# Kernel optimization log

Hardware: AMD Instinct MI355X
Metric: run time of the kernel (lower is better)

## Reference

```python
import jax, jax.numpy as jnp
import numpy as np


def median_pool8(x):
    # x: (N, 1, H0, W0); 8x8 non-overlapping blocks, lower median (torch.median semantics)
    N, C, H0, W0 = x.shape
    H, W = H0 // 8, W0 // 8
    blocks = x.reshape(N, C, H, 8, W, 8).transpose(0, 1, 2, 4, 3, 5).reshape(N, C, H, W, 64)
    return jnp.sort(blocks, axis=-1)[..., (64 - 1) // 2]


def prelu(x, a):
    return jnp.where(x >= 0, x, a * x)


def setup_inputs() -> dict:
    key = jax.random.key(0)
    ks = jax.random.split(key, 12)
    N, C, H, W = 8, 128, 45, 60
    s = 0.05
    return {
        "cnn_encoder_output": jax.random.normal(ks[0], (N, C, H, W), jnp.float32),
        "original_input": jax.random.uniform(ks[1], (N, 4, H * 8, W * 8), jnp.float32),
        "xy": jax.random.normal(ks[2], (N, 2, H * 8, W * 8), jnp.float32),
        # g MLP: two Linear(128,128) + PReLU (single alpha each)
        "g_w0": jax.random.normal(ks[3], (C, C), jnp.float32) * s,
        "g_b0": jnp.zeros((C,), jnp.float32),
        "g_a0": jnp.full((1,), 0.25, jnp.float32),
        "g_w1": jax.random.normal(ks[4], (C, C), jnp.float32) * s,
        "g_b1": jnp.zeros((C,), jnp.float32),
        "g_a1": jnp.full((1,), 0.25, jnp.float32),
        # q update: Linear(256,128) + PReLU
        "q_w": jax.random.normal(ks[5], (C, 2 * C), jnp.float32) * s,
        "q_b": jnp.zeros((C,), jnp.float32),
        "q_a": jnp.full((1,), 0.25, jnp.float32),
        # output conv: Conv2d(256, 128, 3, padding=1)
        "conv_w": jax.random.normal(ks[6], (C, 2 * C, 3, 3), jnp.float32) * s,
        "conv_b": jnp.zeros((C,), jnp.float32),
        "gnn_iterations": 2,
        "k": 16,
        "use_half_precision": 0,
    }


def reference(cnn_encoder_output, original_input, xy,
              g_w0, g_b0, g_a0, g_w1, g_b1, g_a1,
              q_w, q_b, q_a, conv_w, conv_b,
              gnn_iterations, k, use_half_precision):
    N, C, H, W = cnn_encoder_output.shape
    HW = H * W

    # 3D projection: median-pooled x, y, depth -> (N, HW, 3)
    depth = median_pool8(original_input[:, 3:4])
    xc = median_pool8(xy[:, 0:1])
    yc = median_pool8(xy[:, 1:2])
    proj = jnp.concatenate([xc, yc, depth], axis=1).reshape(N, 3, HW).transpose(0, 2, 1)

    # batched KNN: D_ij = sqrt(|pi|^2 + |pj|^2 - 2 pi.pj), k smallest per row
    sq = jnp.sum(proj * proj, axis=-1)                        # (N, HW)
    r = jnp.einsum('nic,njc->nij', proj, proj)                # (N, HW, HW)
    D = jnp.sqrt(jnp.maximum(sq[:, :, None] + sq[:, None, :] - 2.0 * r, 0.0))
    _, knn = jax.lax.top_k(-D, k)                             # (N, HW, K) indices

    h = cnn_encoder_output.transpose(0, 2, 3, 1).reshape(N, HW, C)
    g_params = [(g_w0, g_b0, g_a0), (g_w1, g_b1, g_a1)]

    for _ in range(gnn_iterations):
        # gather neighbor features: (N, HW, K, C)
        nf = jax.vmap(lambda hn, kn: hn[kn])(h, knn)
        for w, b, a in g_params:
            nf = prelu(nf @ w.T + b, a)
        m = jnp.mean(nf, axis=2)                              # (N, HW, C)
        h = prelu(jnp.concatenate([h, m], axis=-1) @ q_w.T + q_b, q_a)

    h_img = h.reshape(N, H, W, C).transpose(0, 3, 1, 2)
    inp = jnp.concatenate([cnn_encoder_output, h_img], axis=1)  # (N, 2C, H, W)
    out = jax.lax.conv_general_dilated(
        inp, conv_w, window_strides=(1, 1), padding=((1, 1), (1, 1)),
        dimension_numbers=('NCHW', 'OIHW', 'NCHW')) + conv_b[None, :, None, None]
    return out
```

## Files before the change

kernel.cpp:

```cpp
#include <hip/hip_runtime.h>
#include <cfloat>
#include <cmath>

#define NB 8
#define CC 128
#define HH 45
#define WW 60
#define HWP 2700
#define KNN 16
#define H0 360
#define W0 480
#define NT 43
#define MROWS 21600

typedef __bf16 bf16_8 __attribute__((ext_vector_type(8)));
typedef __bf16 bf16_4 __attribute__((ext_vector_type(4)));
typedef float  f32x4  __attribute__((ext_vector_type(4)));

__global__ void transpose_cl(const float* __restrict__ in, float* __restrict__ out) {
    __shared__ float tile[32][33];
    int n = blockIdx.z;
    int c0 = blockIdx.y * 32;
    int p0 = blockIdx.x * 32;
    int tx = threadIdx.x & 31, ty = threadIdx.x >> 5;
    #pragma unroll
    for (int r = 0; r < 32; r += 8) {
        int c = c0 + ty + r, p = p0 + tx;
        tile[ty + r][tx] = (p < HWP) ? in[((size_t)n * CC + c) * HWP + p] : 0.f;
    }
    __syncthreads();
    #pragma unroll
    for (int r = 0; r < 32; r += 8) {
        int p = p0 + ty + r, c = c0 + tx;
        if (p < HWP) out[((size_t)n * HWP + p) * CC + c] = tile[tx][ty + r];
    }
}

__global__ void median_pool(const float* __restrict__ xy, const float* __restrict__ orig,
                            float* __restrict__ proj) {
    int w = blockIdx.x * 4 + (threadIdx.x >> 6);
    int lane = threadIdx.x & 63;
    int n = w / (3 * HWP);
    int rem = w % (3 * HWP);
    int c = rem / HWP;
    int b = rem % HWP;
    const float* src = (c < 2) ? (xy + ((size_t)n * 2 + c) * H0 * W0)
                               : (orig + ((size_t)n * 4 + 3) * H0 * W0);
    int by = b / WW, bx = b % WW;
    int r = lane >> 3, col = lane & 7;
    float v = src[(by * 8 + r) * W0 + bx * 8 + col];
    #pragma unroll
    for (int k = 2; k <= 64; k <<= 1) {
        #pragma unroll
        for (int j2 = k >> 1; j2 >= 1; j2 >>= 1) {
            float p = __shfl_xor(v, j2, 64);
            bool dir = (lane & k) == 0;
            bool low = (lane & j2) == 0;
            v = (dir == low) ? fminf(v, p) : fmaxf(v, p);
        }
    }
    if (lane == 31) proj[(size_t)c * (NB * HWP) + (size_t)n * HWP + b] = v;
}

__global__ void __launch_bounds__(512, 6) knn_kernel(const float* __restrict__ proj,
                                                     int* __restrict__ knn) {
#pragma clang fp contract(off)
    __shared__ float4 pts[HWP];
    __shared__ int sbufj[8][64];
    int n = blockIdx.y;
    const float* px = proj + (size_t)n * HWP;
    const float* py = proj + (size_t)NB * HWP + (size_t)n * HWP;
    const float* pz = proj + (size_t)2 * NB * HWP + (size_t)n * HWP;
    for (int t = threadIdx.x; t < HWP; t += 512) {
        float x = px[t], y = py[t], z = pz[t];
        float4 p;
        p.x = x; p.y = y; p.z = z;
        p.w = (x * x + y * y) + z * z;
        pts[t] = p;
    }
    __syncthreads();

    int wave = threadIdx.x >> 6;
    int lane = threadIdx.x & 63;
    int i = blockIdx.x * 8 + wave;
    if (i >= HWP) return;
    float4 pi = pts[i];
    float xi = pi.x, yi = pi.y, zi = pi.z, sqi = pi.w;

    unsigned int sdp[22];
    float mn = FLT_MAX;
    #pragma unroll
    for (int t = 0; t < NT; ++t) {
        int j = lane + t * 64;
        unsigned int u = 0xFFFFu;
        if (j < HWP) {
            float4 pj = pts[j];
            float r = fmaf(zi, pj.z, fmaf(yi, pj.y, xi * pj.x));
            float s = (sqi + pj.w) - 2.0f * r;
            mn = fminf(mn, s);
            float sc = fmaxf(s, 0.f);
            u = (__float_as_uint(sc) + 0xFFFFu) >> 16;
        }
        if (t & 1) sdp[t >> 1] |= (u << 16);
        else       sdp[t >> 1] = u;
    }

    float v = mn;
    #pragma unroll
    for (int k = 2; k <= 64; k <<= 1) {
        #pragma unroll
        for (int j2 = k >> 1; j2 >= 1; j2 >>= 1) {
            float p = __shfl_xor(v, j2, 64);
            bool dir = (lane & k) == 0;
            bool low = (lane & j2) == 0;
            v = (dir == low) ? fminf(v, p) : fmaxf(v, p);
        }
    }
    float M_s = __shfl(v, 15, 64);
    float M_test = (M_s > 0.f) ? (M_s * 1.0000005f + 1e-37f) : 0.0f;
    float M_t2 = M_test * 1.009f;
    unsigned int M_bits = __float_as_uint(M_t2);

    int cnt = 0;
    #pragma unroll
    for (int t = 0; t < NT; ++t) {
        unsigned int u = (t & 1) ? (sdp[t >> 1] >> 16) : (sdp[t >> 1] & 0xFFFFu);
        bool pred = (u << 16) <= M_bits;
        unsigned long long b = __ballot(pred);
        if (b) {
            int off = cnt + (int)__popcll(b & ((1ull << lane) - 1ull));
            if (pred && off < 64) sbufj[wave][off] = lane + t * 64;
            cnt += (int)__popcll(b);
        }
    }

    int myj = 0;
    if (cnt >= KNN && cnt <= 64) {
        unsigned long long key = ~0ull;
        if (lane < cnt) {
            int j = sbufj[wave][lane];
            float4 pj = pts[j];
            float r = fmaf(zi, pj.z, fmaf(yi, pj.y, xi * pj.x));
            float s = (sqi + pj.w) - 2.0f * r;
            float d = sqrtf(fmaxf(s, 0.f));
            key = ((unsigned long long)__float_as_uint(d) << 32) | (unsigned int)j;
        }
        #pragma unroll
        for (int k = 2; k <= 64; k <<= 1) {
            #pragma unroll
            for (int j2 = k >> 1; j2 >= 1; j2 >>= 1) {
                unsigned long long p = __shfl_xor(key, j2, 64);
                bool dir = (lane & k) == 0;
                bool low = (lane & j2) == 0;
                bool keepmin = (dir == low);
                bool pless = p < key;
                key = (pless == keepmin) ? p : key;
            }
        }
        myj = (int)(unsigned int)(key & 0xffffffffull);
    } else {
        float lastd = -FLT_MAX; int lastj = -1;
        #pragma unroll 1
        for (int r = 0; r < KNN; ++r) {
            float bd = FLT_MAX; int bj = 0x7fffffff;
            #pragma unroll 1
            for (int t = 0; t < NT; ++t) {
                int j = lane + t * 64;
                if (j < HWP) {
                    float4 pj = pts[j];
                    float rr = fmaf(zi, pj.z, fmaf(yi, pj.y, xi * pj.x));
                    float s = (sqi + pj.w) - 2.0f * rr;
                    float d = sqrtf(fmaxf(s, 0.f));
                    bool gt = (d > lastd) || (d == lastd && j > lastj);
                    bool lt = (d < bd) || (d == bd && j < bj);
                    if (gt && lt) { bd = d; bj = j; }
                }
            }
            float md = bd; int mj = bj;
            #pragma unroll
            for (int off = 32; off >= 1; off >>= 1) {
                float od = __shfl_xor(md, off, 64);
                int oj = __shfl_xor(mj, off, 64);
                if (od < md || (od == md && oj < mj)) { md = od; mj = oj; }
            }
            if (lane == r) myj = mj;
            lastd = md; lastj = mj;
        }
    }
    if (lane < KNN)
        knn[((size_t)n * HWP + i) * KNN + lane] = myj;
}

template <int K>
__device__ __forceinline__ void wsplit_body(const float* __restrict__ Wt,
                                            __bf16* __restrict__ wh,
                                            __bf16* __restrict__ wl,
                                            int bx, int tid) {
    int t = bx * 256 + tid;
    int j = t & 7;
    int lane = (t >> 3) & 63;
    int nt = (t >> 9) & 7;
    int kc = t >> 12;
    int oc = nt * 16 + (lane & 15);
    int k = kc * 32 + (lane >> 4) * 8 + j;
    float v = Wt[(size_t)oc * K + k];
    __bf16 hi = (__bf16)v;
    wh[t] = hi;
    wl[t] = (__bf16)(v - (float)hi);
}

__global__ void prep_all(const float* __restrict__ g_w0, const float* __restrict__ g_w1,
                         const float* __restrict__ q_w, const float* __restrict__ conv_w,
                         __bf16* __restrict__ g0h, __bf16* __restrict__ g0l,
                         __bf16* __restrict__ g1h, __bf16* __restrict__ g1l,
                         __bf16* __restrict__ qh, __bf16* __restrict__ ql,
                         __bf16* __restrict__ w_frag) {
    int bx = blockIdx.x, tid = threadIdx.x;
    if (bx < 64)        wsplit_body<128>(g_w0, g0h, g0l, bx, tid);
    else if (bx < 128)  wsplit_body<128>(g_w1, g1h, g1l, bx - 64, tid);
    else if (bx < 256)  wsplit_body<256>(q_w, qh, ql, bx - 128, tid);
    else {
        int t = (bx - 256) * 256 + tid;
        int j = t & 7;
        int lane = (t >> 3) & 63;
        int ntile = (t >> 9) & 7;
        int icc = (t >> 12) & 7;
        int tap = t >> 15;
        int oc = ntile * 16 + (lane & 15);
        int ic = icc * 32 + (lane >> 4) * 8 + j;
        w_frag[t] = (__bf16)conv_w[((size_t)oc * 256 + ic) * 9 + tap];
    }
}

__device__ __forceinline__ void layer_32x128(
    const float* __restrict__ src,
    const __bf16* __restrict__ wh, const __bf16* __restrict__ wl,
    int wave, int lane, int kc_base, f32x4 acc[2][2]) {
    int quad = lane >> 4, lm = lane & 15;
    const bf16_8* wh8 = (const bf16_8*)wh;
    const bf16_8* wl8 = (const bf16_8*)wl;
    #pragma unroll
    for (int kc = 0; kc < 4; ++kc) {
        bf16_8 bh[2], bl[2];
        #pragma unroll
        for (int nt = 0; nt < 2; ++nt) {
            const float* p = &src[(nt * 16 + lm) * 132 + kc * 32 + quad * 8];
            float4 v0 = *(const float4*)p;
            float4 v1 = *(const float4*)(p + 4);
            float vs[8] = {v0.x, v0.y, v0.z, v0.w, v1.x, v1.y, v1.z, v1.w};
            #pragma unroll
            for (int e = 0; e < 8; ++e) {
                __bf16 hi = (__bf16)vs[e];
                bh[nt][e] = hi;
                bl[nt][e] = (__bf16)(vs[e] - (float)hi);
            }
        }
        bf16_8 ah[2], al[2];
        #pragma unroll
        for (int mt = 0; mt < 2; ++mt) {
            size_t idx = ((size_t)(kc_base + kc) * 8 + (wave * 2 + mt)) * 64 + lane;
            ah[mt] = wh8[idx];
            al[mt] = wl8[idx];
        }
        #pragma unroll
        for (int mt = 0; mt < 2; ++mt)
            #pragma unroll
            for (int nt = 0; nt < 2; ++nt) {
                acc[mt][nt] = __builtin_amdgcn_mfma_f32_16x16x32_bf16(ah[mt], bh[nt], acc[mt][nt], 0, 0, 0);
                acc[mt][nt] = __builtin_amdgcn_mfma_f32_16x16x32_bf16(ah[mt], bl[nt], acc[mt][nt], 0, 0, 0);
                acc[mt][nt] = __builtin_amdgcn_mfma_f32_16x16x32_bf16(al[mt], bh[nt], acc[mt][nt], 0, 0, 0);
            }
    }
}

__global__ void __launch_bounds__(256) fused_g(
    const float* __restrict__ Ain,
    const __bf16* __restrict__ w0h, const __bf16* __restrict__ w0l,
    const float* __restrict__ b0, const float* __restrict__ a0p,
    const __bf16* __restrict__ w1h, const __bf16* __restrict__ w1l,
    const float* __restrict__ b1, const float* __restrict__ a1p,
    __bf16* __restrict__ tgb) {
    __shared__ float albuf[32 * 132];
    __shared__ float inter[32 * 132];
    int r0 = blockIdx.x * 32;
    int tid = threadIdx.x;
    int wave = tid >> 6, lane = tid & 63;
    int quad = lane >> 4, lm = lane & 15;
    for (int t = tid; t < 1024; t += 256) {
        int row = t >> 5, c4 = (t & 31) * 4;
        *(float4*)&albuf[row * 132 + c4] = *(const float4*)&Ain[(size_t)(r0 + row) * 128 + c4];
    }
    __syncthreads();
    {
        f32x4 acc[2][2] = {};
        layer_32x128(albuf, w0h, w0l, wave, lane, 0, acc);
        float alpha = a0p[0];
        #pragma unroll
        for (int mt = 0; mt < 2; ++mt) {
            int oc0 = wave * 32 + mt * 16 + quad * 4;
            float4 bb = *(const float4*)&b0[oc0];
            float bv[4] = {bb.x, bb.y, bb.z, bb.w};
            #pragma unroll
            for (int nt = 0; nt < 2; ++nt) {
                float4 o;
                float* op = (float*)&o;
                #pragma unroll
                for (int reg = 0; reg < 4; ++reg) {
                    float vv = acc[mt][nt][reg] + bv[reg];
                    op[reg] = (vv >= 0.f) ? vv : alpha * vv;
                }
                *(float4*)&inter[(nt * 16 + lm) * 132 + oc0] = o;
            }
        }
    }
    __syncthreads();
    {
        f32x4 acc[2][2] = {};
        layer_32x128(inter, w1h, w1l, wave, lane, 0, acc);
        float alpha = a1p[0];
        #pragma unroll
        for (int mt = 0; mt < 2; ++mt) {
            int oc0 = wave * 32 + mt * 16 + quad * 4;
            float4 bb = *(const float4*)&b1[oc0];
            float bv[4] = {bb.x, bb.y, bb.z, bb.w};
            #pragma unroll
            for (int nt = 0; nt < 2; ++nt) {
                bf16_4 o;
                #pragma unroll
                for (int reg = 0; reg < 4; ++reg) {
                    float vv = acc[mt][nt][reg] + bv[reg];
                    vv = (vv >= 0.f) ? vv : alpha * vv;
                    o[reg] = (__bf16)vv;
                }
                *(bf16_4*)&tgb[(size_t)(r0 + nt * 16 + lm) * 128 + oc0] = o;
            }
        }
    }
}

__global__ void __launch_bounds__(256) fused_q(
    const float* __restrict__ Ain, const __bf16* __restrict__ tgb,
    const int* __restrict__ knn_idx,
    const __bf16* __restrict__ qh, const __bf16* __restrict__ ql,
    const float* __restrict__ qb, const float* __restrict__ qap,
    float* __restrict__ hout) {
    __shared__ float hlds[32 * 132];
    __shared__ float mlds[32 * 132];
    int r0 = blockIdx.x * 32;
    int tid = threadIdx.x;
    int wave = tid >> 6, lane = tid & 63;
    int quad = lane >> 4, lm = lane & 15;
    for (int t = tid; t < 1024; t += 256) {
        int row = t >> 5, c4 = (t & 31) * 4;
        *(float4*)&hlds[row * 132 + c4] = *(const float4*)&Ain[(size_t)(r0 + row) * 128 + c4];
    }
    {
        int pix = tid >> 3;
        int oct0 = (tid & 7) * 2;
        int grow = r0 + pix;
        int nimg = grow / HWP;
        const int* kn = knn_idx + (size_t)grow * KNN;
        const __bf16* tbase = tgb + ((size_t)nimg * HWP) * 128;
        float a0[8] = {}, a1[8] = {};
        #pragma unroll
        for (int k = 0; k < KNN; ++k) {
            int j = kn[k];
            const __bf16* srcp = tbase + (size_t)j * 128 + oct0 * 8;
            bf16_8 v0 = *(const bf16_8*)srcp;
            bf16_8 v1 = *(const bf16_8*)(srcp + 8);
            #pragma unroll
            for (int e = 0; e < 8; ++e) { a0[e] += (float)v0[e]; a1[e] += (float)v1[e]; }
        }
        const float s = 1.f / 16.f;
        float* dst = &mlds[pix * 132 + oct0 * 8];
        float4 o0 = {a0[0] * s, a0[1] * s, a0[2] * s, a0[3] * s};
        float4 o1 = {a0[4] * s, a0[5] * s, a0[6] * s, a0[7] * s};
        float4 o2 = {a1[0] * s, a1[1] * s, a1[2] * s, a1[3] * s};
        float4 o3 = {a1[4] * s, a1[5] * s, a1[6] * s, a1[7] * s};
        *(float4*)(dst) = o0; *(float4*)(dst + 4) = o1;
        *(float4*)(dst + 8) = o2; *(float4*)(dst + 12) = o3;
    }
    __syncthreads();
    f32x4 acc[2][2] = {};
    layer_32x128(hlds, qh, ql, wave, lane, 0, acc);
    layer_32x128(mlds, qh, ql, wave, lane, 4, acc);
    float alpha = qap[0];
    #pragma unroll
    for (int mt = 0; mt < 2; ++mt) {
        int oc0 = wave * 32 + mt * 16 + quad * 4;
        float4 bb = *(const float4*)&qb[oc0];
        float bv[4] = {bb.x, bb.y, bb.z, bb.w};
        #pragma unroll
        for (int nt = 0; nt < 2; ++nt) {
            float4 o;
            float* op = (float*)&o;
            #pragma unroll
            for (int reg = 0; reg < 4; ++reg) {
                float vv = acc[mt][nt][reg] + bv[reg];
                op[reg] = (vv >= 0.f) ? vv : alpha * vv;
            }
            *(float4*)&hout[(size_t)(r0 + nt * 16 + lm) * 128 + oc0] = o;
        }
    }
}

__global__ void pack_input(const float* __restrict__ cnn_cl, const float* __restrict__ h,
                           __bf16* __restrict__ pad_in) {
    int t = blockIdx.x * 256 + threadIdx.x;
    int cg = t & 31;
    int s = t >> 5;
    int q = s % 68; s /= 68;
    int p = s % 47;
    int n = s / 47;
    int y = p - 1, x = q - 1;
    bf16_8 v = {};
    if (y >= 0 && y < HH && x >= 0 && x < WW) {
        int c0 = cg * 8;
        const float* src = (c0 < 128)
            ? (cnn_cl + (((size_t)n * HWP + y * WW + x) * 128 + c0))
            : (h      + (((size_t)n * HWP + y * WW + x) * 128 + (c0 - 128)));
        float4 l0 = *(const float4*)&src[0];
        float4 l1 = *(const float4*)&src[4];
        v[0] = (__bf16)l0.x; v[1] = (__bf16)l0.y; v[2] = (__bf16)l0.z; v[3] = (__bf16)l0.w;
        v[4] = (__bf16)l1.x; v[5] = (__bf16)l1.y; v[6] = (__bf16)l1.z; v[7] = (__bf16)l1.w;
    }
    ((bf16_8*)pad_in)[t] = v;
}

__global__ void __launch_bounds__(256) conv_mfma(
    const __bf16* __restrict__ pad_in,
    const __bf16* __restrict__ w_frag,
    const float* __restrict__ bias,
    float* __restrict__ out) {
    __shared__ __bf16 alds[3 * 66 * 32];
    int y = blockIdx.x;
    int oh = blockIdx.y;
    int n = blockIdx.z;
    int tid = threadIdx.x;
    int wave = tid >> 6, lane = tid & 63;
    int wm = wave & 1, wq = wave >> 1;
    int quad = lane >> 4, lm = lane & 15;

    f32x4 acc[2][2] = {};
    const bf16_8* wf = (const bf16_8*)w_frag;

    for (int icc = 0; icc < 8; ++icc) {
        __syncthreads();
        for (int t = tid; t < 792; t += 256) {
            int cq = t & 3;
            int xp = (t >> 2) % 66;
            int dy = (t >> 2) / 66;
            size_t src = (((size_t)n * 47 + (y + dy)) * 68 + xp) * 256 + icc * 32 + cq * 8;
            *(bf16_8*)&alds[(dy * 66 + xp) * 32 + cq * 8] = *(const bf16_8*)&pad_in[src];
        }
        __syncthreads();
        #pragma unroll
        for (int tap = 0; tap < 9; ++tap) {
            int ky = tap / 3, kx = tap % 3;
            bf16_8 b[2], a[2];
            #pragma unroll
            for (int nt = 0; nt < 2; ++nt)
                b[nt] = wf[(((tap * 8 + icc) * 8) + (oh * 4 + wq * 2 + nt)) * 64 + lane];
            #pragma unroll
            for (int mt = 0; mt < 2; ++mt)
                a[mt] = *(const bf16_8*)&alds[(ky * 66 + (wm * 32 + mt * 16 + lm + kx)) * 32 + quad * 8];
            #pragma unroll
            for (int mt = 0; mt < 2; ++mt)
                #pragma unroll
                for (int nt = 0; nt < 2; ++nt)
                    acc[mt][nt] = __builtin_amdgcn_mfma_f32_16x16x32_bf16(
                        a[mt], b[nt], acc[mt][nt], 0, 0, 0);
        }
    }
    #pragma unroll
    for (int mt = 0; mt < 2; ++mt) {
        int x0 = wm * 32 + mt * 16 + quad * 4;
        if (x0 >= WW) continue;
        #pragma unroll
        for (int nt = 0; nt < 2; ++nt) {
            int oc = (oh * 4 + wq * 2 + nt) * 16 + lm;
            float bb = bias[oc];
            f32x4 v = acc[mt][nt];
            v[0] += bb; v[1] += bb; v[2] += bb; v[3] += bb;
            *(f32x4*)&out[(((size_t)n * 128 + oc) * HH + y) * WW + x0] = v;
        }
    }
}

extern "C" void kernel_launch(void* const* d_in, const int* in_sizes, int n_in,
                              void* d_out, int out_size, void* d_ws, size_t ws_size,
                              hipStream_t stream) {
    const float* cnn    = (const float*)d_in[0];
    const float* orig   = (const float*)d_in[1];
    const float* xy     = (const float*)d_in[2];
    const float* g_w0   = (const float*)d_in[3];
    const float* g_b0   = (const float*)d_in[4];
    const float* g_a0   = (const float*)d_in[5];
    const float* g_w1   = (const float*)d_in[6];
    const float* g_b1   = (const float*)d_in[7];
    const float* g_a1   = (const float*)d_in[8];
    const float* q_w    = (const float*)d_in[9];
    const float* q_b    = (const float*)d_in[10];
    const float* q_a    = (const float*)d_in[11];
    const float* conv_w = (const float*)d_in[12];
    const float* conv_b = (const float*)d_in[13];
    float* out = (float*)d_out;

    float* ws = (float*)d_ws;
    const size_t S = (size_t)MROWS * CC;
    float*  cnn_cl = ws;
    float*  h      = ws + S;
    float*  base   = ws + 2 * S;
    __bf16* tgb    = (__bf16*)base;
    float*  proj   = base + 1382400;
    int*    knn_i  = (int*)(base + 1382400 + 64800);
    __bf16* wfb    = (__bf16*)(base + 1382400 + 64800 + 345600);
    __bf16* g0h = wfb;            __bf16* g0l = wfb + 16384;
    __bf16* g1h = wfb + 32768;    __bf16* g1l = wfb + 49152;
    __bf16* qh  = wfb + 65536;    __bf16* ql  = wfb + 98304;
    __bf16* w_frag = wfb + 131072;
    __bf16* pad_in = w_frag + 294912;

    transpose_cl<<<dim3(85, 4, NB), 256, 0, stream>>>(cnn, cnn_cl);
    median_pool<<<16200, 256, 0, stream>>>(xy, orig, proj);
    knn_kernel<<<dim3(338, NB), 512, 0, stream>>>(proj, knn_i);
    prep_all<<<1408, 256, 0, stream>>>(g_w0, g_w1, q_w, conv_w,
                                       g0h, g0l, g1h, g1l, qh, ql, w_frag);

    fused_g<<<675, 256, 0, stream>>>(cnn_cl, g0h, g0l, g_b0, g_a0,
                                     g1h, g1l, g_b1, g_a1, tgb);
    fused_q<<<675, 256, 0, stream>>>(cnn_cl, tgb, knn_i, qh, ql, q_b, q_a, h);

    fused_g<<<675, 256, 0, stream>>>(h, g0h, g0l, g_b0, g_a0,
                                     g1h, g1l, g_b1, g_a1, tgb);
    fused_q<<<675, 256, 0, stream>>>(h, tgb, knn_i, qh, ql, q_b, q_a, h);

    pack_input<<<3196, 256, 0, stream>>>(cnn_cl, h, pad_in);
    conv_mfma<<<dim3(HH, 2, NB), 256, 0, stream>>>(pad_in, w_frag, conv_b, out);
}
```

Baseline: 270.3 us.

## Switch GNN MLPs to single bf16 MFMA and write conv input directly

```diff
diff --git a/kernel.cpp b/kernel.cpp
--- a/kernel.cpp
+++ b/kernel.cpp
@@ -17,7 +17,8 @@
 typedef __bf16 bf16_4 __attribute__((ext_vector_type(4)));
 typedef float  f32x4  __attribute__((ext_vector_type(4)));
 
-__global__ void transpose_cl(const float* __restrict__ in, float* __restrict__ out) {
+__global__ void transpose_cl(const float* __restrict__ in, __bf16* __restrict__ cnn_b,
+                             __bf16* __restrict__ pad_in) {
     __shared__ float tile[32][33];
     int n = blockIdx.z;
     int c0 = blockIdx.y * 32;
@@ -32,7 +33,12 @@
     #pragma unroll
     for (int r = 0; r < 32; r += 8) {
         int p = p0 + ty + r, c = c0 + tx;
-        if (p < HWP) out[((size_t)n * HWP + p) * CC + c] = tile[tx][ty + r];
+        if (p < HWP) {
+            __bf16 bv = (__bf16)tile[tx][ty + r];
+            cnn_b[((size_t)n * HWP + p) * 128 + c] = bv;
+            int y = p / WW, x = p % WW;
+            pad_in[(((size_t)n * 47 + y + 1) * 68 + (x + 1)) * 256 + c] = bv;
+        }
     }
 }
 
@@ -67,6 +73,7 @@
 #pragma clang fp contract(off)
     __shared__ float4 pts[HWP];
     __shared__ int sbufj[8][64];
+    __shared__ int scnt[8];
     int n = blockIdx.y;
     const float* px = proj + (size_t)n * HWP;
     const float* py = proj + (size_t)NB * HWP + (size_t)n * HWP;
@@ -121,18 +128,17 @@
     float M_t2 = M_test * 1.009f;
     unsigned int M_bits = __float_as_uint(M_t2);
 
-    int cnt = 0;
+    if (lane == 0) scnt[wave] = 0;
     #pragma unroll
     for (int t = 0; t < NT; ++t) {
         unsigned int u = (t & 1) ? (sdp[t >> 1] >> 16) : (sdp[t >> 1] & 0xFFFFu);
         bool pred = (u << 16) <= M_bits;
-        unsigned long long b = __ballot(pred);
-        if (b) {
-            int off = cnt + (int)__popcll(b & ((1ull << lane) - 1ull));
-            if (pred && off < 64) sbufj[wave][off] = lane + t * 64;
-            cnt += (int)__popcll(b);
-        }
-    }
+        if (pred) {
+            int slot = atomicAdd(&scnt[wave], 1);
+            if (slot < 64) sbufj[wave][slot] = lane + t * 64;
+        }
+    }
+    int cnt = scnt[wave];
 
     int myj = 0;
     if (cnt >= KNN && cnt <= 64) {
@@ -192,10 +198,8 @@
 }
 
 template <int K>
-__device__ __forceinline__ void wsplit_body(const float* __restrict__ Wt,
-                                            __bf16* __restrict__ wh,
-                                            __bf16* __restrict__ wl,
-                                            int bx, int tid) {
+__device__ __forceinline__ void wfrag_body(const float* __restrict__ Wt,
+                                           __bf16* __restrict__ wf, int bx, int tid) {
     int t = bx * 256 + tid;
     int j = t & 7;
     int lane = (t >> 3) & 63;
@@ -203,22 +207,17 @@
     int kc = t >> 12;
     int oc = nt * 16 + (lane & 15);
     int k = kc * 32 + (lane >> 4) * 8 + j;
-    float v = Wt[(size_t)oc * K + k];
-    __bf16 hi = (__bf16)v;
-    wh[t] = hi;
-    wl[t] = (__bf16)(v - (float)hi);
+    wf[t] = (__bf16)Wt[(size_t)oc * K + k];
 }
 
 __global__ void prep_all(const float* __restrict__ g_w0, const float* __restrict__ g_w1,
                          const float* __restrict__ q_w, const float* __restrict__ conv_w,
-                         __bf16* __restrict__ g0h, __bf16* __restrict__ g0l,
-                         __bf16* __restrict__ g1h, __bf16* __restrict__ g1l,
-                         __bf16* __restrict__ qh, __bf16* __restrict__ ql,
-                         __bf16* __restrict__ w_frag) {
+                         __bf16* __restrict__ g0f, __bf16* __restrict__ g1f,
+                         __bf16* __restrict__ qf, __bf16* __restrict__ w_frag) {
     int bx = blockIdx.x, tid = threadIdx.x;
-    if (bx < 64)        wsplit_body<128>(g_w0, g0h, g0l, bx, tid);
-    else if (bx < 128)  wsplit_body<128>(g_w1, g1h, g1l, bx - 64, tid);
-    else if (bx < 256)  wsplit_body<256>(q_w, qh, ql, bx - 128, tid);
+    if (bx < 64)        wfrag_body<128>(g_w0, g0f, bx, tid);
+    else if (bx < 128)  wfrag_body<128>(g_w1, g1f, bx - 64, tid);
+    else if (bx < 256)  wfrag_body<256>(q_w, qf, bx - 128, tid);
     else {
         int t = (bx - 256) * 256 + tid;
         int j = t & 7;
@@ -232,68 +231,51 @@
     }
 }
 
-__device__ __forceinline__ void layer_32x128(
-    const float* __restrict__ src,
-    const __bf16* __restrict__ wh, const __bf16* __restrict__ wl,
+__device__ __forceinline__ void layer_b(
+    const __bf16* __restrict__ src,
+    const __bf16* __restrict__ wf,
     int wave, int lane, int kc_base, f32x4 acc[2][2]) {
     int quad = lane >> 4, lm = lane & 15;
-    const bf16_8* wh8 = (const bf16_8*)wh;
-    const bf16_8* wl8 = (const bf16_8*)wl;
+    const bf16_8* wf8 = (const bf16_8*)wf;
     #pragma unroll
     for (int kc = 0; kc < 4; ++kc) {
-        bf16_8 bh[2], bl[2];
-        #pragma unroll
-        for (int nt = 0; nt < 2; ++nt) {
-            const float* p = &src[(nt * 16 + lm) * 132 + kc * 32 + quad * 8];
-            float4 v0 = *(const float4*)p;
-            float4 v1 = *(const float4*)(p + 4);
-            float vs[8] = {v0.x, v0.y, v0.z, v0.w, v1.x, v1.y, v1.z, v1.w};
-            #pragma unroll
-            for (int e = 0; e < 8; ++e) {
-                __bf16 hi = (__bf16)vs[e];
-                bh[nt][e] = hi;
-                bl[nt][e] = (__bf16)(vs[e] - (float)hi);
-            }
-        }
-        bf16_8 ah[2], al[2];
-        #pragma unroll
-        for (int mt = 0; mt < 2; ++mt) {
-            size_t idx = ((size_t)(kc_base + kc) * 8 + (wave * 2 + mt)) * 64 + lane;
-            ah[mt] = wh8[idx];
-            al[mt] = wl8[idx];
-        }
+        bf16_8 b[2], a[2];
+        #pragma unroll
+        for (int nt = 0; nt < 2; ++nt)
+            b[nt] = *(const bf16_8*)&src[(nt * 16 + lm) * 136 + kc * 32 + quad * 8];
         #pragma unroll
         for (int mt = 0; mt < 2; ++mt)
-            #pragma unroll
-            for (int nt = 0; nt < 2; ++nt) {
-                acc[mt][nt] = __builtin_amdgcn_mfma_f32_16x16x32_bf16(ah[mt], bh[nt], acc[mt][nt], 0, 0, 0);
-                acc[mt][nt] = __builtin_amdgcn_mfma_f32_16x16x32_bf16(ah[mt], bl[nt], acc[mt][nt], 0, 0, 0);
-                acc[mt][nt] = __builtin_amdgcn_mfma_f32_16x16x32_bf16(al[mt], bh[nt], acc[mt][nt], 0, 0, 0);
-            }
+            a[mt] = wf8[((size_t)(kc_base + kc) * 8 + (wave * 2 + mt)) * 64 + lane];
+        #pragma unroll
+        for (int mt = 0; mt < 2; ++mt)
+            #pragma unroll
+            for (int nt = 0; nt < 2; ++nt)
+                acc[mt][nt] = __builtin_amdgcn_mfma_f32_16x16x32_bf16(
+                    a[mt], b[nt], acc[mt][nt], 0, 0, 0);
     }
 }
 
 __global__ void __launch_bounds__(256) fused_g(
-    const float* __restrict__ Ain,
-    const __bf16* __restrict__ w0h, const __bf16* __restrict__ w0l,
-    const float* __restrict__ b0, const float* __restrict__ a0p,
-    const __bf16* __restrict__ w1h, const __bf16* __restrict__ w1l,
-    const float* __restrict__ b1, const float* __restrict__ a1p,
+    const __bf16* __restrict__ Ain,
+    const __bf16* __restrict__ w0f, const float* __restrict__ b0, const float* __restrict__ a0p,
+    const __bf16* __restrict__ w1f, const float* __restrict__ b1, const float* __restrict__ a1p,
     __bf16* __restrict__ tgb) {
-    __shared__ float albuf[32 * 132];
-    __shared__ float inter[32 * 132];
+    __shared__ __bf16 albuf[32 * 136];
+    __shared__ __bf16 inter[32 * 136];
     int r0 = blockIdx.x * 32;
     int tid = threadIdx.x;
     int wave = tid >> 6, lane = tid & 63;
     int quad = lane >> 4, lm = lane & 15;
-    for (int t = tid; t < 1024; t += 256) {
-        int row = t >> 5, c4 = (t & 31) * 4;
-        *(float4*)&albuf[row * 132 + c4] = *(const float4*)&Ain[(size_t)(r0 + row) * 128 + c4];
+    #pragma unroll
+    for (int t = tid; t < 512; t += 256) {
+        int row = t >> 4, c8 = (t & 15) * 8;
+        *(bf16_8*)&albuf[row * 136 + c8] =
+            *(const bf16_8*)&Ain[(size_t)(r0 + row) * 128 + c8];
     }
     __syncthreads();
     {
         f32x4 acc[2][2] = {};
-        layer_32x128(albuf, w0h, w0l, wave, lane, 0, acc);
+        layer_b(albuf, w0f, wave, lane, 0, acc);
         float alpha = a0p[0];
         #pragma unroll
         for (int mt = 0; mt < 2; ++mt) {
@@ -302,21 +284,21 @@
             float bv[4] = {bb.x, bb.y, bb.z, bb.w};
             #pragma unroll
             for (int nt = 0; nt < 2; ++nt) {
-                float4 o;
-                float* op = (float*)&o;
+                bf16_4 o;
                 #pragma unroll
                 for (int reg = 0; reg < 4; ++reg) {
                     float vv = acc[mt][nt][reg] + bv[reg];
-                    op[reg] = (vv >= 0.f) ? vv : alpha * vv;
+                    vv = (vv >= 0.f) ? vv : alpha * vv;
+                    o[reg] = (__bf16)vv;
                 }
-                *(float4*)&inter[(nt * 16 + lm) * 132 + oc0] = o;
+                *(bf16_4*)&inter[(nt * 16 + lm) * 136 + oc0] = o;
             }
         }
     }
     __syncthreads();
     {
         f32x4 acc[2][2] = {};
-        layer_32x128(inter, w1h, w1l, wave, lane, 0, acc);
+        layer_b(inter, w1f, wave, lane, 0, acc);
         float alpha = a1p[0];
         #pragma unroll
         for (int mt = 0; mt < 2; ++mt) {
@@ -339,20 +321,22 @@
 }
 
 __global__ void __launch_bounds__(256) fused_q(
-    const float* __restrict__ Ain, const __bf16* __restrict__ tgb,
+    const __bf16* __restrict__ Ain, const __bf16* __restrict__ tgb,
     const int* __restrict__ knn_idx,
-    const __bf16* __restrict__ qh, const __bf16* __restrict__ ql,
-    const float* __restrict__ qb, const float* __restrict__ qap,
-    float* __restrict__ hout) {
-    __shared__ float hlds[32 * 132];
-    __shared__ float mlds[32 * 132];
+    const __bf16* __restrict__ qf, const float* __restrict__ qb,
+    const float* __restrict__ qap,
+    __bf16* __restrict__ out_lin, __bf16* __restrict__ pad_out, int mode) {
+    __shared__ __bf16 hlds[32 * 136];
+    __shared__ __bf16 mlds[32 * 136];
     int r0 = blockIdx.x * 32;
     int tid = threadIdx.x;
     int wave = tid >> 6, lane = tid & 63;
     int quad = lane >> 4, lm = lane & 15;
-    for (int t = tid; t < 1024; t += 256) {
-        int row = t >> 5, c4 = (t & 31) * 4;
-        *(float4*)&hlds[row * 132 + c4] = *(const float4*)&Ain[(size_t)(r0 + row) * 128 + c4];
+    #pragma unroll
+    for (int t = tid; t < 512; t += 256) {
+        int row = t >> 4, c8 = (t & 15) * 8;
+        *(bf16_8*)&hlds[row * 136 + c8] =
+            *(const bf16_8*)&Ain[(size_t)(r0 + row) * 128 + c8];
     }
     {
         int pix = tid >> 3;
@@ -372,18 +356,16 @@
             for (int e = 0; e < 8; ++e) { a0[e] += (float)v0[e]; a1[e] += (float)v1[e]; }
         }
         const float s = 1.f / 16.f;
-        float* dst = &mlds[pix * 132 + oct0 * 8];
-        float4 o0 = {a0[0] * s, a0[1] * s, a0[2] * s, a0[3] * s};
-        float4 o1 = {a0[4] * s, a0[5] * s, a0[6] * s, a0[7] * s};
-        float4 o2 = {a1[0] * s, a1[1] * s, a1[2] * s, a1[3] * s};
-        float4 o3 = {a1[4] * s, a1[5] * s, a1[6] * s, a1[7] * s};
-        *(float4*)(dst) = o0; *(float4*)(dst + 4) = o1;
-        *(float4*)(dst + 8) = o2; *(float4*)(dst + 12) = o3;
+        bf16_8 o0, o1;
+        #pragma unroll
+        for (int e = 0; e < 8; ++e) { o0[e] = (__bf16)(a0[e] * s); o1[e] = (__bf16)(a1[e] * s); }
+        *(bf16_8*)&mlds[pix * 136 + oct0 * 8] = o0;
+        *(bf16_8*)&mlds[pix * 136 + oct0 * 8 + 8] = o1;
     }
     __syncthreads();
     f32x4 acc[2][2] = {};
-    layer_32x128(hlds, qh, ql, wave, lane, 0, acc);
-    layer_32x128(mlds, qh, ql, wave, lane, 4, acc);
+    layer_b(hlds, qf, wave, lane, 0, acc);
+    layer_b(mlds, qf, wave, lane, 4, acc);
     float alpha = qap[0];
     #pragma unroll
     for (int mt = 0; mt < 2; ++mt) {
@@ -392,39 +374,41 @@
         float bv[4] = {bb.x, bb.y, bb.z, bb.w};
         #pragma unroll
         for (int nt = 0; nt < 2; ++nt) {
-            float4 o;
-            float* op = (float*)&o;
+            bf16_4 o;
             #pragma unroll
             for (int reg = 0; reg < 4; ++reg) {
                 float vv = acc[mt][nt][reg] + bv[reg];
-                op[reg] = (vv >= 0.f) ? vv : alpha * vv;
-            }
-            *(float4*)&hout[(size_t)(r0 + nt * 16 + lm) * 128 + oc0] = o;
-        }
-    }
-}
-
-__global__ void pack_input(const float* __restrict__ cnn_cl, const float* __restrict__ h,
-                           __bf16* __restrict__ pad_in) {
+                vv = (vv >= 0.f) ? vv : alpha * vv;
+                o[reg] = (__bf16)vv;
+            }
+            int grow = r0 + nt * 16 + lm;
+            if (mode == 0) {
+                *(bf16_4*)&out_lin[(size_t)grow * 128 + oc0] = o;
+            } else {
+                int n = grow / HWP, p = grow % HWP;
+                int y = p / WW, x = p % WW;
+                *(bf16_4*)&pad_out[(((size_t)n * 47 + y + 1) * 68 + (x + 1)) * 256 + 128 + oc0] = o;
+            }
+        }
+    }
+}
+
+__global__ void zero_border(__bf16* __restrict__ pad_in) {
     int t = blockIdx.x * 256 + threadIdx.x;
     int cg = t & 31;
     int s = t >> 5;
-    int q = s % 68; s /= 68;
-    int p = s % 47;
-    int n = s / 47;
-    int y = p - 1, x = q - 1;
-    bf16_8 v = {};
-    if (y >= 0 && y < HH && x >= 0 && x < WW) {
-        int c0 = cg * 8;
-        const float* src = (c0 < 128)
-            ? (cnn_cl + (((size_t)n * HWP + y * WW + x) * 128 + c0))
-            : (h      + (((size_t)n * HWP + y * WW + x) * 128 + (c0 - 128)));
-        float4 l0 = *(const float4*)&src[0];
-        float4 l1 = *(const float4*)&src[4];
-        v[0] = (__bf16)l0.x; v[1] = (__bf16)l0.y; v[2] = (__bf16)l0.z; v[3] = (__bf16)l0.w;
-        v[4] = (__bf16)l1.x; v[5] = (__bf16)l1.y; v[6] = (__bf16)l1.z; v[7] = (__bf16)l1.w;
-    }
-    ((bf16_8*)pad_in)[t] = v;
+    int cell = s % 496;
+    int n = s / 496;
+    int y, x;
+    if (cell < 136) { y = (cell < 68) ? 0 : 46; x = cell % 68; }
+    else {
+        int rem = cell - 136;
+        y = 1 + rem / 8;
+        int k = rem % 8;
+        x = (k == 0) ? 0 : (60 + k);
+    }
+    bf16_8 z = {};
+    *(bf16_8*)&pad_in[(((size_t)n * 47 + y) * 68 + x) * 256 + cg * 8] = z;
 }
 
 __global__ void __launch_bounds__(256) conv_mfma(
@@ -507,34 +491,29 @@
     float* out = (float*)d_out;
 
     float* ws = (float*)d_ws;
-    const size_t S = (size_t)MROWS * CC;
-    float*  cnn_cl = ws;
-    float*  h      = ws + S;
-    float*  base   = ws + 2 * S;
-    __bf16* tgb    = (__bf16*)base;
-    float*  proj   = base + 1382400;
-    int*    knn_i  = (int*)(base + 1382400 + 64800);
-    __bf16* wfb    = (__bf16*)(base + 1382400 + 64800 + 345600);
-    __bf16* g0h = wfb;            __bf16* g0l = wfb + 16384;
-    __bf16* g1h = wfb + 32768;    __bf16* g1l = wfb + 49152;
-    __bf16* qh  = wfb + 65536;    __bf16* ql  = wfb + 98304;
-    __bf16* w_frag = wfb + 131072;
+    const size_t SB = (size_t)MROWS * 128;
+    __bf16* cnn_b  = (__bf16*)ws;
+    __bf16* h_b    = cnn_b + SB;
+    __bf16* tgb    = h_b + SB;
+    float*  proj   = (float*)(tgb + SB);
+    int*    knn_i  = (int*)(proj + 64800);
+    __bf16* g0f    = (__bf16*)(knn_i + (size_t)MROWS * KNN);
+    __bf16* g1f    = g0f + 16384;
+    __bf16* qf     = g1f + 16384;
+    __bf16* w_frag = qf + 32768;
     __bf16* pad_in = w_frag + 294912;
 
-    transpose_cl<<<dim3(85, 4, NB), 256, 0, stream>>>(cnn, cnn_cl);
+    transpose_cl<<<dim3(85, 4, NB), 256, 0, stream>>>(cnn, cnn_b, pad_in);
     median_pool<<<16200, 256, 0, stream>>>(xy, orig, proj);
     knn_kernel<<<dim3(338, NB), 512, 0, stream>>>(proj, knn_i);
-    prep_all<<<1408, 256, 0, stream>>>(g_w0, g_w1, q_w, conv_w,
-                                       g0h, g0l, g1h, g1l, qh, ql, w_frag);
-
-    fused_g<<<675, 256, 0, stream>>>(cnn_cl, g0h, g0l, g_b0, g_a0,
-                                     g1h, g1l, g_b1, g_a1, tgb);
-    fused_q<<<675, 256, 0, stream>>>(cnn_cl, tgb, knn_i, qh, ql, q_b, q_a, h);
-
-    fused_g<<<675, 256, 0, stream>>>(h, g0h, g0l, g_b0, g_a0,
-                                     g1h, g1l, g_b1, g_a1, tgb);
-    fused_q<<<675, 256, 0, stream>>>(h, tgb, knn_i, qh, ql, q_b, q_a, h);
-
-    pack_input<<<3196, 256, 0, stream>>>(cnn_cl, h, pad_in);
+    prep_all<<<1408, 256, 0, stream>>>(g_w0, g_w1, q_w, conv_w, g0f, g1f, qf, w_frag);
+    zero_border<<<496, 256, 0, stream>>>(pad_in);
+
+    fused_g<<<675, 256, 0, stream>>>(cnn_b, g0f, g_b0, g_a0, g1f, g_b1, g_a1, tgb);
+    fused_q<<<675, 256, 0, stream>>>(cnn_b, tgb, knn_i, qf, q_b, q_a, h_b, pad_in, 0);
+
+    fused_g<<<675, 256, 0, stream>>>(h_b, g0f, g_b0, g_a0, g1f, g_b1, g_a1, tgb);
+    fused_q<<<675, 256, 0, stream>>>(h_b, tgb, knn_i, qf, q_b, q_a, h_b, pad_in, 1);
+
     conv_mfma<<<dim3(HH, 2, NB), 256, 0, stream>>>(pad_in, w_frag, conv_b, out);
 }
```

Result: faster. 254.0 us (-6.0%).
